# Optimization experiments

Measured on AMD Instinct MI355X. Metric: run time of the kernel, lower is better.

## Reference

```python
import jax, jax.numpy as jnp
import numpy as np

XYZ, DIRS, APP = 63, 27, 0
HID, OUT, NLAYERS, SKIPS = 256, 4, 8, (4,)

def _linear_init(key, fan_in, fan_out):
    kw, kb = jax.random.split(key)
    s = 1.0 / np.sqrt(fan_in)
    W = jax.random.uniform(kw, (fan_in, fan_out), jnp.float32, -s, s)
    b = jax.random.uniform(kb, (fan_out,), jnp.float32, -s, s)
    return W, b

def setup_inputs() -> dict:
    key = jax.random.key(0)
    keys = jax.random.split(key, NLAYERS + 2)
    x = jax.random.normal(keys[0], (262144, XYZ + DIRS + APP), jnp.float32)
    d = {"x": x}
    in_dim = XYZ
    for i in range(NLAYERS):
        # skip-concat: layer after a skip index sees hid+xyz inputs
        fan_in = HID + XYZ if (i - 1) in SKIPS else (XYZ if i == 0 else HID)
        W, b = _linear_init(keys[i + 1], fan_in, HID)
        d[f"W{i}"], d[f"b{i}"] = W, b
    Wout, bout = _linear_init(keys[-1], HID, OUT)
    d["Wout"], d["bout"] = Wout, bout
    return d

def reference(x, W0, b0, W1, b1, W2, b2, W3, b3, W4, b4, W5, b5, W6, b6, W7, b7, Wout, bout):
    Ws = [W0, W1, W2, W3, W4, W5, W6, W7]
    bs = [b0, b1, b2, b3, b4, b5, b6, b7]
    input_pts = x[..., :XYZ]  # dirs/app split off but unused (use_viewdirs=False)
    h = input_pts
    for i in range(NLAYERS):
        h = jax.nn.relu(h @ Ws[i] + bs[i])
        if i in SKIPS:
            h = jnp.concatenate([input_pts, h], axis=-1)
    return h @ Wout + bout  # [N, 4] = rgb + density logits
```

## Files before the change

### kernel.cpp

```cpp
#include <hip/hip_runtime.h>


typedef _Float16 h8 __attribute__((ext_vector_type(8)));
typedef float f4 __attribute__((ext_vector_type(4)));

#define OFF_L0   0
#define OFF_L1   16384
#define OFF_L2   81920
#define OFF_L3   147456
#define OFF_L4   212992
#define OFF_L5   278528
#define OFF_L6   360448
#define OFF_L7   425984
#define OFF_OUT  491520
#define TOT_HALVES 495616
#define TOT_GROUPS (TOT_HALVES / 8)

__global__ void nerf_prep(const float* __restrict__ W0, const float* __restrict__ W1,
                          const float* __restrict__ W2, const float* __restrict__ W3,
                          const float* __restrict__ W4, const float* __restrict__ W5,
                          const float* __restrict__ W6, const float* __restrict__ W7,
                          const float* __restrict__ Wout, _Float16* __restrict__ wf)
{
    int g = blockIdx.x * 256 + threadIdx.x;
    if (g >= TOT_GROUPS) return;

    const int bounds[10] = {0, 2048, 10240, 18432, 26624, 34816, 45056, 53248, 61440, 61952};
    const float* Ws[9] = {W0, W1, W2, W3, W4, W5, W6, W7, Wout};

    int L = 0;
    while (L < 8 && g >= bounds[L + 1]) ++L;

    int t    = g - bounds[L];
    int lane = t & 63;
    int q    = t >> 6;
    int NF   = (L == 8) ? 1 : 16;
    int nf   = q % NF;
    int ks   = q / NF;
    int n    = nf * 16 + (lane & 15);
    int k0   = ks * 32 + (lane >> 4) * 8;

    const float* W = Ws[L];
    h8 v;
#pragma unroll
    for (int i = 0; i < 8; ++i) {
        int k = k0 + i;
        float val = 0.f;
        if (L == 0) {
            if (k < 63) val = W[k * 256 + n];
        } else if (L == 5) {
            if (k < 256)             val = W[(63 + k) * 256 + n];
            else if ((k - 256) < 63) val = W[(k - 256) * 256 + n];
        } else if (L == 8) {
            if (n < 4) val = W[k * 4 + n];
        } else {
            val = W[k * 256 + n];
        }
        v[i] = (_Float16)val;
    }
    *(h8*)(wf + (size_t)g * 8) = v;
}

__device__ __forceinline__ const h8* bfrag_ptr(const _Float16* __restrict__ w,
                                               int ks, int wid, int nf, int lane)
{
    return (const h8*)(w + (size_t)((ks * 16 + (wid * 4 + nf)) * 64 + lane) * 8);
}

__device__ __forceinline__ void barrier_nodrain()
{
    asm volatile("s_waitcnt lgkmcnt(0)" ::: "memory");
    __builtin_amdgcn_s_barrier();
    __builtin_amdgcn_sched_barrier(0);
}

template <int KSTEPS, int MODE, int GB3, bool LAST>
__device__ __forceinline__ void mlp_layer(const _Float16 (&rbuf)[64][264],
                                          _Float16 (&wbuf)[64][264],
                                          const _Float16 (&xbuf)[64][72],
                                          const _Float16* __restrict__ wfrag,
                                          const _Float16* __restrict__ wnext,
                                          const float* __restrict__ bias,
                                          int wid, int lane, h8 (&pf)[3][4])
{
    const int lg = lane >> 4, ln = lane & 15;

    f4 bv[4];
#pragma unroll
    for (int cf = 0; cf < 4; ++cf)
        bv[cf] = *(const f4*)&bias[wid * 64 + cf * 16 + lg * 4];

    f4 acc[4][4];
#pragma unroll
    for (int cf = 0; cf < 4; ++cf)
#pragma unroll
        for (int sf = 0; sf < 4; ++sf)
            acc[cf][sf] = bv[cf];

#pragma unroll
    for (int ks = 0; ks < KSTEPS; ++ks) {
        const int slot = (GB3 + ks) % 3;
        __builtin_amdgcn_s_setprio(1);
        h8 hfr[4];
#pragma unroll
        for (int sf = 0; sf < 4; ++sf) {
            const _Float16* ap;
            if constexpr (MODE == 1) {
                ap = &xbuf[sf * 16 + ln][ks * 32 + lg * 8];
            } else if constexpr (MODE == 2) {
                ap = (ks < 8) ? &rbuf[sf * 16 + ln][ks * 32 + lg * 8]
                              : &xbuf[sf * 16 + ln][(ks - 8) * 32 + lg * 8];
            } else {
                ap = &rbuf[sf * 16 + ln][ks * 32 + lg * 8];
            }
            hfr[sf] = *(const h8*)ap;
        }
#pragma unroll
        for (int cf = 0; cf < 4; ++cf)
#pragma unroll
            for (int sf = 0; sf < 4; ++sf)
                acc[cf][sf] = __builtin_amdgcn_mfma_f32_16x16x32_f16(pf[slot][cf], hfr[sf], acc[cf][sf], 0, 0, 0);
        __builtin_amdgcn_s_setprio(0);
        if (ks + 3 < KSTEPS) {
#pragma unroll
            for (int cf = 0; cf < 4; ++cf)
                pf[slot][cf] = *bfrag_ptr(wfrag, ks + 3, wid, cf, lane);
        } else {
            if constexpr (!LAST) {
#pragma unroll
                for (int cf = 0; cf < 4; ++cf)
                    pf[slot][cf] = *bfrag_ptr(wnext, ks + 3 - KSTEPS, wid, cf, lane);
            }
        }
    }

#pragma unroll
    for (int cf = 0; cf < 4; ++cf) {
#pragma unroll
        for (int sf = 0; sf < 4; ++sf) {
            union { _Float16 h[4]; unsigned long long u; } p;
#pragma unroll
            for (int i = 0; i < 4; ++i)
                p.h[i] = (_Float16)fmaxf(acc[cf][sf][i], 0.f);
            *(unsigned long long*)&wbuf[sf * 16 + ln][wid * 64 + cf * 16 + lg * 4] = p.u;
        }
    }
    barrier_nodrain();
}

__global__ __launch_bounds__(256, 2) void nerf_fused(
    const float* __restrict__ x,
    const float* __restrict__ b0, const float* __restrict__ b1, const float* __restrict__ b2,
    const float* __restrict__ b3, const float* __restrict__ b4, const float* __restrict__ b5,
    const float* __restrict__ b6, const float* __restrict__ b7, const float* __restrict__ bout,
    const _Float16* __restrict__ wf,
    float* __restrict__ out)
{
    __shared__ _Float16 hb[2][64][264];
    __shared__ _Float16 xbuf[64][72];

    const int tid  = threadIdx.x;
    const int wid  = tid >> 6;
    const int lane = tid & 63;
    const int lg   = lane >> 4, ln = lane & 15;
    const int row0 = blockIdx.x * 64;

    h8 pf[3][4];
#pragma unroll
    for (int cf = 0; cf < 4; ++cf) {
        pf[0][cf] = *bfrag_ptr(wf + OFF_L0, 0, wid, cf, lane);
        pf[1][cf] = *bfrag_ptr(wf + OFF_L0, 1, wid, cf, lane);
        pf[2][cf] = *bfrag_ptr(wf + OFF_L1, 0, wid, cf, lane);
    }

    for (int idx = tid; idx < 64 * 64; idx += 256) {
        int r = idx >> 6, c = idx & 63;
        float v = (c < 63) ? x[(size_t)(row0 + r) * 90 + c] : 0.f;
        xbuf[r][c] = (_Float16)v;
    }
    barrier_nodrain();

    mlp_layer<2,  1, 0, false>(hb[0], hb[0], xbuf, wf + OFF_L0, wf + OFF_L1, b0, wid, lane, pf);
    mlp_layer<8,  0, 2, false>(hb[0], hb[1], xbuf, wf + OFF_L1, wf + OFF_L2, b1, wid, lane, pf);
    mlp_layer<8,  0, 1, false>(hb[1], hb[0], xbuf, wf + OFF_L2, wf + OFF_L3, b2, wid, lane, pf);
    mlp_layer<8,  0, 0, false>(hb[0], hb[1], xbuf, wf + OFF_L3, wf + OFF_L4, b3, wid, lane, pf);
    mlp_layer<8,  0, 2, false>(hb[1], hb[0], xbuf, wf + OFF_L4, wf + OFF_L5, b4, wid, lane, pf);
    mlp_layer<10, 2, 1, false>(hb[0], hb[1], xbuf, wf + OFF_L5, wf + OFF_L6, b5, wid, lane, pf);
    mlp_layer<8,  0, 2, false>(hb[1], hb[0], xbuf, wf + OFF_L6, wf + OFF_L7, b6, wid, lane, pf);
    mlp_layer<8,  0, 1, true >(hb[0], hb[1], xbuf, wf + OFF_L7, wf + OFF_L7, b7, wid, lane, pf);

    f4 oacc;
#pragma unroll
    for (int i = 0; i < 4; ++i) oacc[i] = 0.f;
#pragma unroll
    for (int ks = 0; ks < 8; ++ks) {
        h8 bfr = *(const h8*)(wf + OFF_OUT + (size_t)(ks * 64 + lane) * 8);
        h8 afr = *(const h8*)&hb[1][wid * 16 + ln][ks * 32 + lg * 8];
        oacc = __builtin_amdgcn_mfma_f32_16x16x32_f16(afr, bfr, oacc, 0, 0, 0);
    }
    if (ln < 4) {
        float bo = bout[ln];
#pragma unroll
        for (int i = 0; i < 4; ++i) {
            int r = row0 + wid * 16 + lg * 4 + i;
            out[(size_t)r * 4 + ln] = oacc[i] + bo;
        }
    }
}

extern "C" void kernel_launch(void* const* d_in, const int* in_sizes, int n_in,
                              void* d_out, int out_size, void* d_ws, size_t ws_size,
                              hipStream_t stream)
{
    const float* x = (const float*)d_in[0];
    const float* W[9];
    const float* b[9];
    for (int i = 0; i < 8; ++i) {
        W[i] = (const float*)d_in[1 + 2 * i];
        b[i] = (const float*)d_in[2 + 2 * i];
    }
    W[8] = (const float*)d_in[17];
    b[8] = (const float*)d_in[18];

    _Float16* wf = (_Float16*)d_ws;

    nerf_prep<<<(TOT_GROUPS + 255) / 256, 256, 0, stream>>>(
        W[0], W[1], W[2], W[3], W[4], W[5], W[6], W[7], W[8], wf);

    nerf_fused<<<262144 / 64, 256, 0, stream>>>(
        x, b[0], b[1], b[2], b[3], b[4], b[5], b[6], b[7], b[8], wf,
        (float*)d_out);
}
```

Baseline: 241.2 us.

## Double rows per block, use single XOR-swizzled LDS buffer, two-slot weight prefetch

Each block now processes 128 rows instead of 64, so every weight fragment loaded from global memory feeds twice as many MFMAs. The ping-pong activation buffers with padded rows are replaced by one XOR-swizzled buffer that is overwritten in place after an extra barrier, which avoids bank conflicts without padding and keeps LDS usage within budget. The weight prefetch drops from three slots to two to make room for the doubled accumulators (128 fp32 values per lane). The risks are heavy register pressure under launch_bounds(256,2), an extra barrier per layer, and half as many blocks to spread across the CUs.

```diff
diff --git a/kernel.cpp b/kernel.cpp
--- a/kernel.cpp
+++ b/kernel.cpp
@@ -67,6 +67,19 @@
     return (const h8*)(w + (size_t)((ks * 16 + (wid * 4 + nf)) * 64 + lane) * 8);
 }
 
+__device__ __forceinline__ char* hgen(_Float16* h, int row, int col)
+{
+    int byte = (row << 9) + (col << 1);
+    byte ^= (row & 7) << 4;
+    return (char*)h + byte;
+}
+__device__ __forceinline__ char* xgen(_Float16* xb, int row, int col)
+{
+    int byte = (row << 7) + (col << 1);
+    byte ^= (row & 7) << 4;
+    return (char*)xb + byte;
+}
+
 __device__ __forceinline__ void barrier_nodrain()
 {
     asm volatile("s_waitcnt lgkmcnt(0)" ::: "memory");
@@ -74,14 +87,12 @@
     __builtin_amdgcn_sched_barrier(0);
 }
 
-template <int KSTEPS, int MODE, int GB3, bool LAST>
-__device__ __forceinline__ void mlp_layer(const _Float16 (&rbuf)[64][264],
-                                          _Float16 (&wbuf)[64][264],
-                                          const _Float16 (&xbuf)[64][72],
+template <int KSTEPS, int MODE, bool LAST>
+__device__ __forceinline__ void mlp_layer(_Float16* hbuf, _Float16* xbuf,
                                           const _Float16* __restrict__ wfrag,
                                           const _Float16* __restrict__ wnext,
                                           const float* __restrict__ bias,
-                                          int wid, int lane, h8 (&pf)[3][4])
+                                          int wid, int lane, h8 (&pf)[2][4])
 {
     const int lg = lane >> 4, ln = lane & 15;
 
@@ -90,59 +101,57 @@
     for (int cf = 0; cf < 4; ++cf)
         bv[cf] = *(const f4*)&bias[wid * 64 + cf * 16 + lg * 4];
 
-    f4 acc[4][4];
+    f4 acc[4][8];
 #pragma unroll
     for (int cf = 0; cf < 4; ++cf)
 #pragma unroll
-        for (int sf = 0; sf < 4; ++sf)
+        for (int sf = 0; sf < 8; ++sf)
             acc[cf][sf] = bv[cf];
 
 #pragma unroll
     for (int ks = 0; ks < KSTEPS; ++ks) {
-        const int slot = (GB3 + ks) % 3;
         __builtin_amdgcn_s_setprio(1);
-        h8 hfr[4];
-#pragma unroll
-        for (int sf = 0; sf < 4; ++sf) {
-            const _Float16* ap;
+#pragma unroll
+        for (int sf = 0; sf < 8; ++sf) {
+            const char* ap;
             if constexpr (MODE == 1) {
-                ap = &xbuf[sf * 16 + ln][ks * 32 + lg * 8];
+                ap = xgen(xbuf, sf * 16 + ln, ks * 32 + lg * 8);
             } else if constexpr (MODE == 2) {
-                ap = (ks < 8) ? &rbuf[sf * 16 + ln][ks * 32 + lg * 8]
-                              : &xbuf[sf * 16 + ln][(ks - 8) * 32 + lg * 8];
+                ap = (ks < 8) ? hgen(hbuf, sf * 16 + ln, ks * 32 + lg * 8)
+                              : xgen(xbuf, sf * 16 + ln, (ks - 8) * 32 + lg * 8);
             } else {
-                ap = &rbuf[sf * 16 + ln][ks * 32 + lg * 8];
+                ap = hgen(hbuf, sf * 16 + ln, ks * 32 + lg * 8);
             }
-            hfr[sf] = *(const h8*)ap;
-        }
-#pragma unroll
-        for (int cf = 0; cf < 4; ++cf)
-#pragma unroll
-            for (int sf = 0; sf < 4; ++sf)
-                acc[cf][sf] = __builtin_amdgcn_mfma_f32_16x16x32_f16(pf[slot][cf], hfr[sf], acc[cf][sf], 0, 0, 0);
+            h8 hfr = *(const h8*)ap;
+#pragma unroll
+            for (int cf = 0; cf < 4; ++cf)
+                acc[cf][sf] = __builtin_amdgcn_mfma_f32_16x16x32_f16(pf[ks & 1][cf], hfr, acc[cf][sf], 0, 0, 0);
+        }
         __builtin_amdgcn_s_setprio(0);
-        if (ks + 3 < KSTEPS) {
+        if (ks + 2 < KSTEPS) {
 #pragma unroll
             for (int cf = 0; cf < 4; ++cf)
-                pf[slot][cf] = *bfrag_ptr(wfrag, ks + 3, wid, cf, lane);
+                pf[ks & 1][cf] = *bfrag_ptr(wfrag, ks + 2, wid, cf, lane);
         } else {
             if constexpr (!LAST) {
 #pragma unroll
                 for (int cf = 0; cf < 4; ++cf)
-                    pf[slot][cf] = *bfrag_ptr(wnext, ks + 3 - KSTEPS, wid, cf, lane);
+                    pf[ks & 1][cf] = *bfrag_ptr(wnext, ks + 2 - KSTEPS, wid, cf, lane);
             }
         }
     }
 
+    barrier_nodrain();
+
 #pragma unroll
     for (int cf = 0; cf < 4; ++cf) {
 #pragma unroll
-        for (int sf = 0; sf < 4; ++sf) {
+        for (int sf = 0; sf < 8; ++sf) {
             union { _Float16 h[4]; unsigned long long u; } p;
 #pragma unroll
             for (int i = 0; i < 4; ++i)
                 p.h[i] = (_Float16)fmaxf(acc[cf][sf][i], 0.f);
-            *(unsigned long long*)&wbuf[sf * 16 + ln][wid * 64 + cf * 16 + lg * 4] = p.u;
+            *(unsigned long long*)hgen(hbuf, sf * 16 + ln, wid * 64 + cf * 16 + lg * 4) = p.u;
         }
     }
     barrier_nodrain();
@@ -156,54 +165,56 @@
     const _Float16* __restrict__ wf,
     float* __restrict__ out)
 {
-    __shared__ _Float16 hb[2][64][264];
-    __shared__ _Float16 xbuf[64][72];
+    __shared__ _Float16 hbuf[128 * 256];
+    __shared__ _Float16 xbuf[128 * 64];
 
     const int tid  = threadIdx.x;
     const int wid  = tid >> 6;
     const int lane = tid & 63;
     const int lg   = lane >> 4, ln = lane & 15;
-    const int row0 = blockIdx.x * 64;
-
-    h8 pf[3][4];
-#pragma unroll
-    for (int cf = 0; cf < 4; ++cf) {
-        pf[0][cf] = *bfrag_ptr(wf + OFF_L0, 0, wid, cf, lane);
-        pf[1][cf] = *bfrag_ptr(wf + OFF_L0, 1, wid, cf, lane);
-        pf[2][cf] = *bfrag_ptr(wf + OFF_L1, 0, wid, cf, lane);
-    }
-
-    for (int idx = tid; idx < 64 * 64; idx += 256) {
+    const int row0 = blockIdx.x * 128;
+
+    h8 pf[2][4];
+#pragma unroll
+    for (int s = 0; s < 2; ++s)
+#pragma unroll
+        for (int cf = 0; cf < 4; ++cf)
+            pf[s][cf] = *bfrag_ptr(wf + OFF_L0, s, wid, cf, lane);
+
+    for (int idx = tid; idx < 128 * 64; idx += 256) {
         int r = idx >> 6, c = idx & 63;
         float v = (c < 63) ? x[(size_t)(row0 + r) * 90 + c] : 0.f;
-        xbuf[r][c] = (_Float16)v;
+        *(_Float16*)xgen(xbuf, r, c) = (_Float16)v;
     }
     barrier_nodrain();
 
-    mlp_layer<2,  1, 0, false>(hb[0], hb[0], xbuf, wf + OFF_L0, wf + OFF_L1, b0, wid, lane, pf);
-    mlp_layer<8,  0, 2, false>(hb[0], hb[1], xbuf, wf + OFF_L1, wf + OFF_L2, b1, wid, lane, pf);
-    mlp_layer<8,  0, 1, false>(hb[1], hb[0], xbuf, wf + OFF_L2, wf + OFF_L3, b2, wid, lane, pf);
-    mlp_layer<8,  0, 0, false>(hb[0], hb[1], xbuf, wf + OFF_L3, wf + OFF_L4, b3, wid, lane, pf);
-    mlp_layer<8,  0, 2, false>(hb[1], hb[0], xbuf, wf + OFF_L4, wf + OFF_L5, b4, wid, lane, pf);
-    mlp_layer<10, 2, 1, false>(hb[0], hb[1], xbuf, wf + OFF_L5, wf + OFF_L6, b5, wid, lane, pf);
-    mlp_layer<8,  0, 2, false>(hb[1], hb[0], xbuf, wf + OFF_L6, wf + OFF_L7, b6, wid, lane, pf);
-    mlp_layer<8,  0, 1, true >(hb[0], hb[1], xbuf, wf + OFF_L7, wf + OFF_L7, b7, wid, lane, pf);
-
-    f4 oacc;
-#pragma unroll
-    for (int i = 0; i < 4; ++i) oacc[i] = 0.f;
-#pragma unroll
-    for (int ks = 0; ks < 8; ++ks) {
-        h8 bfr = *(const h8*)(wf + OFF_OUT + (size_t)(ks * 64 + lane) * 8);
-        h8 afr = *(const h8*)&hb[1][wid * 16 + ln][ks * 32 + lg * 8];
-        oacc = __builtin_amdgcn_mfma_f32_16x16x32_f16(afr, bfr, oacc, 0, 0, 0);
-    }
-    if (ln < 4) {
-        float bo = bout[ln];
-#pragma unroll
-        for (int i = 0; i < 4; ++i) {
-            int r = row0 + wid * 16 + lg * 4 + i;
-            out[(size_t)r * 4 + ln] = oacc[i] + bo;
+    mlp_layer<2,  1, false>(hbuf, xbuf, wf + OFF_L0, wf + OFF_L1, b0, wid, lane, pf);
+    mlp_layer<8,  0, false>(hbuf, xbuf, wf + OFF_L1, wf + OFF_L2, b1, wid, lane, pf);
+    mlp_layer<8,  0, false>(hbuf, xbuf, wf + OFF_L2, wf + OFF_L3, b2, wid, lane, pf);
+    mlp_layer<8,  0, false>(hbuf, xbuf, wf + OFF_L3, wf + OFF_L4, b3, wid, lane, pf);
+    mlp_layer<8,  0, false>(hbuf, xbuf, wf + OFF_L4, wf + OFF_L5, b4, wid, lane, pf);
+    mlp_layer<10, 2, false>(hbuf, xbuf, wf + OFF_L5, wf + OFF_L6, b5, wid, lane, pf);
+    mlp_layer<8,  0, false>(hbuf, xbuf, wf + OFF_L6, wf + OFF_L7, b6, wid, lane, pf);
+    mlp_layer<8,  0, true >(hbuf, xbuf, wf + OFF_L7, wf + OFF_L7, b7, wid, lane, pf);
+
+#pragma unroll
+    for (int half = 0; half < 2; ++half) {
+        f4 oacc;
+#pragma unroll
+        for (int i = 0; i < 4; ++i) oacc[i] = 0.f;
+#pragma unroll
+        for (int ks = 0; ks < 8; ++ks) {
+            h8 bfr = *(const h8*)(wf + OFF_OUT + (size_t)(ks * 64 + lane) * 8);
+            h8 afr = *(const h8*)hgen(hbuf, wid * 32 + half * 16 + ln, ks * 32 + lg * 8);
+            oacc = __builtin_amdgcn_mfma_f32_16x16x32_f16(afr, bfr, oacc, 0, 0, 0);
+        }
+        if (ln < 4) {
+            float bo = bout[ln];
+#pragma unroll
+            for (int i = 0; i < 4; ++i) {
+                int r = row0 + wid * 32 + half * 16 + lg * 4 + i;
+                out[(size_t)r * 4 + ln] = oacc[i] + bo;
+            }
         }
     }
 }
@@ -227,7 +238,7 @@
     nerf_prep<<<(TOT_GROUPS + 255) / 256, 256, 0, stream>>>(
         W[0], W[1], W[2], W[3], W[4], W[5], W[6], W[7], W[8], wf);
 
-    nerf_fused<<<262144 / 64, 256, 0, stream>>>(
+    nerf_fused<<<262144 / 128, 256, 0, stream>>>(
         x, b[0], b[1], b[2], b[3], b[4], b[5], b[6], b[7], b[8], wf,
         (float*)d_out);
 }
```

After: 371.6 us. 1.54x slower.
